# Kernel optimization log

Hardware: AMD Instinct MI355X
Metric: run time of the kernel (lower is better)

The kernel has to match this reference:

```python
import jax, jax.numpy as jnp
import numpy as np

B, H, S, D = 2, 8, 2048, 64
N_HASHES = 6
EPS = 1e-8


def setup_inputs() -> dict:
    key = jax.random.key(0)
    kq, kk, kv, kr = jax.random.split(key, 4)
    Q = jax.random.normal(kq, (B, H, S, D), dtype=jnp.float32)
    K = jax.random.normal(kk, (B, H, S, D), dtype=jnp.float32)
    V = jax.random.normal(kv, (B, H, S, D), dtype=jnp.float32)
    rotations = jax.random.normal(kr, (H, N_HASHES, D), dtype=jnp.float32)
    return {"Q": Q, "K": K, "V": V, "rotations": rotations}


def _buckets(X, rotations, powers):
    # X: [b,h,l,d] -> integer bucket id per position, [b,h,l]
    Xn = X / (jnp.linalg.norm(X, axis=-1, keepdims=True) + 1e-8)
    bits = jnp.einsum('bhld,hnd->bhln', Xn, rotations) > 0
    return jnp.sum(bits.astype(jnp.int32) * powers, axis=-1)


def reference(Q, K, V, rotations):
    n_hashes = rotations.shape[1]
    d = Q.shape[-1]
    powers = (2 ** jnp.arange(n_hashes)).astype(jnp.int32)
    q_buckets = _buckets(Q, rotations, powers)  # [b,h,sq]
    k_buckets = _buckets(K, rotations, powers)  # [b,h,sk]
    # queries only attend to keys whose full hash code matches exactly
    match = q_buckets[..., :, None] == k_buckets[..., None, :]  # [b,h,sq,sk]
    scores = jnp.einsum('bhqd,bhkd->bhqk', Q, K) / (d ** 0.5)
    row_has = jnp.any(match, axis=-1, keepdims=True)
    masked = jnp.where(match, scores, -jnp.inf)
    m = jnp.max(masked, axis=-1, keepdims=True)
    m = jnp.where(row_has, m, 0.0)  # avoid -inf for empty rows
    e = jnp.where(match, jnp.exp(scores - m), 0.0)
    weights = e / (jnp.sum(e, axis=-1, keepdims=True) + EPS)
    out = jnp.einsum('bhqk,bhkd->bhqd', weights, V)
    return out / n_hashes
```

## Files before the change

kernel.cpp:

```cpp
#include <hip/hip_runtime.h>
#include <math.h>


constexpr int S_LEN = 2048;
constexpr int D = 64;
constexpr int NHASH = 6;
constexpr int BH = 16;
constexpr int NB = 64;
constexpr int QPAD = 4;
constexpr int PADQ = S_LEN + (QPAD - 1) * NB;
constexpr int NGRP = PADQ / QPAD;
constexpr int NBLK = NGRP / 4;
constexpr int GSTRIDE = 37;
constexpr size_t KTP_OFF = 1u << 20;

__global__ __launch_bounds__(256) void lsh_buckets2(const float* __restrict__ Q,
                                                    const float* __restrict__ K,
                                                    const float* __restrict__ rot,
                                                    int* __restrict__ qb,
                                                    int* __restrict__ kb) {
    const int gw   = (blockIdx.x * 256 + threadIdx.x) >> 6;
    const int lane = threadIdx.x & 63;
    const bool isK = gw >= BH * S_LEN;
    const int wid  = isK ? gw - BH * S_LEN : gw;
    const float* X = isK ? K : Q;
    int* dst       = isK ? kb : qb;
    const int h    = (wid >> 11) & 7;

    const float x  = X[(size_t)wid * D + lane];
    const float* r = rot + (size_t)h * NHASH * D + lane;
    float p0 = x * r[0 * D], p1 = x * r[1 * D], p2 = x * r[2 * D];
    float p3 = x * r[3 * D], p4 = x * r[4 * D], p5 = x * r[5 * D];
#pragma unroll
    for (int off = 32; off >= 1; off >>= 1) {
        p0 += __shfl_xor(p0, off, 64);
        p1 += __shfl_xor(p1, off, 64);
        p2 += __shfl_xor(p2, off, 64);
        p3 += __shfl_xor(p3, off, 64);
        p4 += __shfl_xor(p4, off, 64);
        p5 += __shfl_xor(p5, off, 64);
    }
    int bucket = (p0 > 0.f ? 1 : 0) | (p1 > 0.f ? 2 : 0) | (p2 > 0.f ? 4 : 0) |
                 (p3 > 0.f ? 8 : 0) | (p4 > 0.f ? 16 : 0) | (p5 > 0.f ? 32 : 0);
    if (lane == 0) dst[wid] = bucket;
}

__global__ __launch_bounds__(256) void lsh_sortfuse_bh(const int* __restrict__ qbuckets,
                                                       const int* __restrict__ kbuckets,
                                                       int* __restrict__ q_plist,
                                                       int* __restrict__ k_list) {
    __shared__ int hist[NB];
    __shared__ int cur[NB];
    __shared__ int kst[NB], kcnt[NB];
    __shared__ int qst[NB];
    __shared__ int total;
    const int bh  = blockIdx.x;
    const int tid = threadIdx.x;

    if (tid < NB) hist[tid] = 0;
    __syncthreads();
    int myk[8];
#pragma unroll
    for (int i = 0; i < 8; ++i) {
        myk[i] = kbuckets[bh * S_LEN + i * 256 + tid];
        atomicAdd(&hist[myk[i]], 1);
    }
    __syncthreads();
    if (tid < NB) {
        const int cnt = hist[tid];
        int x = cnt;
#pragma unroll
        for (int off = 1; off < 64; off <<= 1) {
            const int y = __shfl_up(x, off, 64);
            if (tid >= off) x += y;
        }
        kst[tid]  = x - cnt;
        kcnt[tid] = cnt;
        cur[tid]  = x - cnt;
    }
    __syncthreads();
    {
        int* klp = k_list + bh * S_LEN;
#pragma unroll
        for (int i = 0; i < 8; ++i) {
            const int b    = myk[i];
            const int slot = atomicAdd(&cur[b], 1);
            klp[slot] = i * 256 + tid;
        }
    }
    __syncthreads();

    if (tid < NB) hist[tid] = 0;
    __syncthreads();
    int myq[8];
#pragma unroll
    for (int i = 0; i < 8; ++i) {
        myq[i] = qbuckets[bh * S_LEN + i * 256 + tid];
        atomicAdd(&hist[myq[i]], 1);
    }
    __syncthreads();
    if (tid < NB) {
        const int cnt = hist[tid];
        const int v   = (cnt + QPAD - 1) & ~(QPAD - 1);
        int x = v;
#pragma unroll
        for (int off = 1; off < 64; off <<= 1) {
            const int y = __shfl_up(x, off, 64);
            if (tid >= off) x += y;
        }
        qst[tid] = x - v;
        cur[tid] = x - v;
        if (tid == 63) total = x;
    }
    __syncthreads();

    int* qp = q_plist + bh * PADQ;
    if (tid < NB) {
        const int cnt    = hist[tid];
        const int padded = (cnt + QPAD - 1) & ~(QPAD - 1);
        const int sent   = 0xFFFF | (kcnt[tid] << 16);
        for (int t = qst[tid] + cnt; t < qst[tid] + padded; ++t) qp[t] = sent;
    }
    for (int t = total + tid; t < PADQ; t += 256) qp[t] = -1;
#pragma unroll
    for (int i = 0; i < 8; ++i) {
        const int b    = myq[i];
        const int slot = atomicAdd(&cur[b], 1);
        const int pos  = slot & 3;
        int e = i * 256 + tid;
        if (pos == 0)      e |= kst[b] << 16;
        else if (pos == 1) e |= kcnt[b] << 16;
        qp[slot] = e;
    }
}

__global__ __launch_bounds__(256) void lsh_kpack(const float* __restrict__ K,
                                                 const int* __restrict__ k_list,
                                                 float* __restrict__ Ktp) {
    const int gw   = (blockIdx.x * 256 + threadIdx.x) >> 6;
    const int lane = threadIdx.x & 63;
    const int bh   = gw >> 9;
    const int s0   = (gw & 511) * 4;
    const float* Kb = K + (size_t)bh * S_LEN * D;
    const int* kl   = k_list + bh * S_LEN;
    float* kt       = Ktp + (size_t)bh * 16 * S_LEN * 4;
    const int dblk  = lane >> 2, dj = lane & 3;
#pragma unroll
    for (int j = 0; j < 4; ++j) {
        const int slot = s0 + j;
        const int kidx = kl[slot];
        const float v  = Kb[(size_t)kidx * D + lane];
        kt[((size_t)dblk * S_LEN + slot) * 4 + dj] = v;
    }
}

__global__ __launch_bounds__(256) void lsh_attn_p(const float* __restrict__ Q,
                                                  const float* __restrict__ V,
                                                  const float* __restrict__ Ktp,
                                                  const int* __restrict__ q_plist,
                                                  const int* __restrict__ k_list,
                                                  float* __restrict__ out) {
    __shared__ float wbuf[4][QPAD][64];
    __shared__ int   kbuf[4][64];

    const int wv   = threadIdx.x >> 6;
    const int lane = threadIdx.x & 63;
    const int w    = blockIdx.x;
    const int bh   = (w & 7) + 8 * ((w >> 3) & 1);
    const int gb   = ((w >> 4) * GSTRIDE) % NBLK;
    const int grp  = gb * 4 + wv;

    const int* pl = q_plist + bh * PADQ + 4 * grp;
    const int e0 = __builtin_amdgcn_readfirstlane(pl[0]);
    if ((e0 & 0xFFFF) == 0xFFFF) return;
    const int e1 = __builtin_amdgcn_readfirstlane(pl[1]);
    const int e2 = __builtin_amdgcn_readfirstlane(pl[2]);
    const int e3 = __builtin_amdgcn_readfirstlane(pl[3]);

    const int q0 = e0 & 0xFFFF;
    const int ks = (unsigned)e0 >> 16;
    const int nk = (unsigned)e1 >> 16;
    const int t1 = e1 & 0xFFFF, t2 = e2 & 0xFFFF, t3 = e3 & 0xFFFF;
    const bool v1 = t1 != 0xFFFF, v2 = t2 != 0xFFFF, v3 = t3 != 0xFFFF;
    const int q1 = v1 ? t1 : q0;
    const int q2 = v2 ? t2 : q0;
    const int q3 = v3 ? t3 : q0;

    float* outb = out + (size_t)bh * S_LEN * D;
    if (nk == 0) {
        outb[(size_t)q0 * D + lane] = 0.0f;
        if (v1) outb[(size_t)q1 * D + lane] = 0.0f;
        if (v2) outb[(size_t)q2 * D + lane] = 0.0f;
        if (v3) outb[(size_t)q3 * D + lane] = 0.0f;
        return;
    }

    const int* kl     = k_list + bh * S_LEN + ks;
    const float* ktb  = Ktp + (size_t)bh * 16 * S_LEN * 4;
    const float* Vb   = V + (size_t)bh * S_LEN * D;
    const float* qr0  = Q + ((size_t)bh * S_LEN + q0) * D;
    const float* qr1  = Q + ((size_t)bh * S_LEN + q1) * D;
    const float* qr2  = Q + ((size_t)bh * S_LEN + q2) * D;
    const float* qr3  = Q + ((size_t)bh * S_LEN + q3) * D;

    float l0 = 0.f, l1 = 0.f, l2 = 0.f, l3 = 0.f;
    float acc0 = 0.f, acc1 = 0.f, acc2 = 0.f, acc3 = 0.f;

    for (int c = 0; c * 64 < nk; ++c) {
        const int cnk  = min(64, nk - c * 64);
        const int cl   = min(lane, cnk - 1);
        const int kidx = kl[c * 64 + cl];
        const int slot = ks + c * 64 + cl;

        float s0 = 0.f, s1 = 0.f, s2 = 0.f, s3 = 0.f;
#pragma unroll
        for (int d4 = 0; d4 < 16; ++d4) {
            const float4 kv = *(const float4*)(ktb + ((size_t)d4 * S_LEN + slot) * 4);
            const float4 a  = *(const float4*)(qr0 + d4 * 4);
            const float4 b  = *(const float4*)(qr1 + d4 * 4);
            const float4 cq = *(const float4*)(qr2 + d4 * 4);
            const float4 dq = *(const float4*)(qr3 + d4 * 4);
            s0 += a.x * kv.x + a.y * kv.y + a.z * kv.z + a.w * kv.w;
            s1 += b.x * kv.x + b.y * kv.y + b.z * kv.z + b.w * kv.w;
            s2 += cq.x * kv.x + cq.y * kv.y + cq.z * kv.z + cq.w * kv.w;
            s3 += dq.x * kv.x + dq.y * kv.y + dq.z * kv.z + dq.w * kv.w;
        }

        const bool kvalid = lane < cnk;
        const float ea = kvalid ? __expf(s0 * 0.125f) : 0.f;
        const float eb = kvalid ? __expf(s1 * 0.125f) : 0.f;
        const float ec = kvalid ? __expf(s2 * 0.125f) : 0.f;
        const float ed = kvalid ? __expf(s3 * 0.125f) : 0.f;
        l0 += ea; l1 += eb; l2 += ec; l3 += ed;
        wbuf[wv][0][lane] = ea;
        wbuf[wv][1][lane] = eb;
        wbuf[wv][2][lane] = ec;
        wbuf[wv][3][lane] = ed;
        kbuf[wv][lane]    = kidx;

        const int ng = (cnk + 3) >> 2;
        for (int g = 0; g < ng; ++g) {
            const int4   kk = *(const int4*)&kbuf[wv][g * 4];
            const float4 eA = *(const float4*)&wbuf[wv][0][g * 4];
            const float4 eB = *(const float4*)&wbuf[wv][1][g * 4];
            const float4 eC = *(const float4*)&wbuf[wv][2][g * 4];
            const float4 eD = *(const float4*)&wbuf[wv][3][g * 4];
            const float vx = Vb[(size_t)kk.x * D + lane];
            const float vy = Vb[(size_t)kk.y * D + lane];
            const float vz = Vb[(size_t)kk.z * D + lane];
            const float vw = Vb[(size_t)kk.w * D + lane];
            acc0 += eA.x * vx + eA.y * vy + eA.z * vz + eA.w * vw;
            acc1 += eB.x * vx + eB.y * vy + eB.z * vz + eB.w * vw;
            acc2 += eC.x * vx + eC.y * vy + eC.z * vz + eC.w * vw;
            acc3 += eD.x * vx + eD.y * vy + eD.z * vz + eD.w * vw;
        }
    }

#pragma unroll
    for (int off = 32; off >= 1; off >>= 1) {
        l0 += __shfl_xor(l0, off, 64);
        l1 += __shfl_xor(l1, off, 64);
        l2 += __shfl_xor(l2, off, 64);
        l3 += __shfl_xor(l3, off, 64);
    }

    const float inv6 = 1.0f / 6.0f;
    outb[(size_t)q0 * D + lane] = acc0 / (l0 + 1e-8f) * inv6;
    if (v1) outb[(size_t)q1 * D + lane] = acc1 / (l1 + 1e-8f) * inv6;
    if (v2) outb[(size_t)q2 * D + lane] = acc2 / (l2 + 1e-8f) * inv6;
    if (v3) outb[(size_t)q3 * D + lane] = acc3 / (l3 + 1e-8f) * inv6;
}

__global__ __launch_bounds__(256) void lsh_attn_g(const float* __restrict__ Q,
                                                  const float* __restrict__ K,
                                                  const float* __restrict__ V,
                                                  const int* __restrict__ q_plist,
                                                  const int* __restrict__ k_list,
                                                  float* __restrict__ out) {
    __shared__ float wbuf[4][QPAD][64];
    __shared__ int   kbuf[4][64];

    const int wv   = threadIdx.x >> 6;
    const int lane = threadIdx.x & 63;
    const int w    = blockIdx.x;
    const int bh   = (w & 7) + 8 * ((w >> 3) & 1);
    const int gb   = ((w >> 4) * GSTRIDE) % NBLK;
    const int grp  = gb * 4 + wv;

    const int* pl = q_plist + bh * PADQ + 4 * grp;
    const int e0 = __builtin_amdgcn_readfirstlane(pl[0]);
    if ((e0 & 0xFFFF) == 0xFFFF) return;
    const int e1 = __builtin_amdgcn_readfirstlane(pl[1]);
    const int e2 = __builtin_amdgcn_readfirstlane(pl[2]);
    const int e3 = __builtin_amdgcn_readfirstlane(pl[3]);

    const int q0 = e0 & 0xFFFF;
    const int ks = (unsigned)e0 >> 16;
    const int nk = (unsigned)e1 >> 16;
    const int t1 = e1 & 0xFFFF, t2 = e2 & 0xFFFF, t3 = e3 & 0xFFFF;
    const bool v1 = t1 != 0xFFFF, v2 = t2 != 0xFFFF, v3 = t3 != 0xFFFF;
    const int q1 = v1 ? t1 : q0;
    const int q2 = v2 ? t2 : q0;
    const int q3 = v3 ? t3 : q0;

    float* outb = out + (size_t)bh * S_LEN * D;
    if (nk == 0) {
        outb[(size_t)q0 * D + lane] = 0.0f;
        if (v1) outb[(size_t)q1 * D + lane] = 0.0f;
        if (v2) outb[(size_t)q2 * D + lane] = 0.0f;
        if (v3) outb[(size_t)q3 * D + lane] = 0.0f;
        return;
    }

    const int* kl     = k_list + bh * S_LEN + ks;
    const float* Kb   = K + (size_t)bh * S_LEN * D;
    const float* Vb   = V + (size_t)bh * S_LEN * D;
    const float* qr0  = Q + ((size_t)bh * S_LEN + q0) * D;
    const float* qr1  = Q + ((size_t)bh * S_LEN + q1) * D;
    const float* qr2  = Q + ((size_t)bh * S_LEN + q2) * D;
    const float* qr3  = Q + ((size_t)bh * S_LEN + q3) * D;

    float l0 = 0.f, l1 = 0.f, l2 = 0.f, l3 = 0.f;
    float acc0 = 0.f, acc1 = 0.f, acc2 = 0.f, acc3 = 0.f;

    for (int c = 0; c * 64 < nk; ++c) {
        const int cnk  = min(64, nk - c * 64);
        const int kidx = kl[c * 64 + min(lane, cnk - 1)];
        const float* krow = Kb + (size_t)kidx * D;

        float s0 = 0.f, s1 = 0.f, s2 = 0.f, s3 = 0.f;
#pragma unroll
        for (int d4 = 0; d4 < 16; ++d4) {
            const float4 kv = *(const float4*)(krow + d4 * 4);
            const float4 a  = *(const float4*)(qr0 + d4 * 4);
            const float4 b  = *(const float4*)(qr1 + d4 * 4);
            const float4 cq = *(const float4*)(qr2 + d4 * 4);
            const float4 dq = *(const float4*)(qr3 + d4 * 4);
            s0 += a.x * kv.x + a.y * kv.y + a.z * kv.z + a.w * kv.w;
            s1 += b.x * kv.x + b.y * kv.y + b.z * kv.z + b.w * kv.w;
            s2 += cq.x * kv.x + cq.y * kv.y + cq.z * kv.z + cq.w * kv.w;
            s3 += dq.x * kv.x + dq.y * kv.y + dq.z * kv.z + dq.w * kv.w;
        }

        const bool kvalid = lane < cnk;
        const float ea = kvalid ? __expf(s0 * 0.125f) : 0.f;
        const float eb = kvalid ? __expf(s1 * 0.125f) : 0.f;
        const float ec = kvalid ? __expf(s2 * 0.125f) : 0.f;
        const float ed = kvalid ? __expf(s3 * 0.125f) : 0.f;
        l0 += ea; l1 += eb; l2 += ec; l3 += ed;
        wbuf[wv][0][lane] = ea;
        wbuf[wv][1][lane] = eb;
        wbuf[wv][2][lane] = ec;
        wbuf[wv][3][lane] = ed;
        kbuf[wv][lane]    = kidx;

        const int ng = (cnk + 3) >> 2;
        for (int g = 0; g < ng; ++g) {
            const int4   kk = *(const int4*)&kbuf[wv][g * 4];
            const float4 eA = *(const float4*)&wbuf[wv][0][g * 4];
            const float4 eB = *(const float4*)&wbuf[wv][1][g * 4];
            const float4 eC = *(const float4*)&wbuf[wv][2][g * 4];
            const float4 eD = *(const float4*)&wbuf[wv][3][g * 4];
            const float vx = Vb[(size_t)kk.x * D + lane];
            const float vy = Vb[(size_t)kk.y * D + lane];
            const float vz = Vb[(size_t)kk.z * D + lane];
            const float vw = Vb[(size_t)kk.w * D + lane];
            acc0 += eA.x * vx + eA.y * vy + eA.z * vz + eA.w * vw;
            acc1 += eB.x * vx + eB.y * vy + eB.z * vz + eB.w * vw;
            acc2 += eC.x * vx + eC.y * vy + eC.z * vz + eC.w * vw;
            acc3 += eD.x * vx + eD.y * vy + eD.z * vz + eD.w * vw;
        }
    }

#pragma unroll
    for (int off = 32; off >= 1; off >>= 1) {
        l0 += __shfl_xor(l0, off, 64);
        l1 += __shfl_xor(l1, off, 64);
        l2 += __shfl_xor(l2, off, 64);
        l3 += __shfl_xor(l3, off, 64);
    }

    const float inv6 = 1.0f / 6.0f;
    outb[(size_t)q0 * D + lane] = acc0 / (l0 + 1e-8f) * inv6;
    if (v1) outb[(size_t)q1 * D + lane] = acc1 / (l1 + 1e-8f) * inv6;
    if (v2) outb[(size_t)q2 * D + lane] = acc2 / (l2 + 1e-8f) * inv6;
    if (v3) outb[(size_t)q3 * D + lane] = acc3 / (l3 + 1e-8f) * inv6;
}

extern "C" void kernel_launch(void* const* d_in, const int* in_sizes, int n_in,
                              void* d_out, int out_size, void* d_ws, size_t ws_size,
                              hipStream_t stream) {
    const float* Q   = (const float*)d_in[0];
    const float* K   = (const float*)d_in[1];
    const float* V   = (const float*)d_in[2];
    const float* rot = (const float*)d_in[3];
    float* out = (float*)d_out;

    char* ws = (char*)d_ws;
    int* q_buckets = (int*)(ws);
    int* k_buckets = (int*)(ws + 131072);
    int* k_list    = (int*)(ws + 262144);
    int* q_plist   = (int*)(ws + 393216);
    float* Ktp     = (float*)(ws + KTP_OFF);

    const size_t ktp_bytes = (size_t)BH * 16 * S_LEN * 4 * sizeof(float);
    const bool packed = ws_size >= KTP_OFF + ktp_bytes;

    lsh_buckets2<<<2 * BH * S_LEN / 4, 256, 0, stream>>>(Q, K, rot, q_buckets, k_buckets);
    lsh_sortfuse_bh<<<BH, 256, 0, stream>>>(q_buckets, k_buckets, q_plist, k_list);
    if (packed) {
        lsh_kpack<<<BH * S_LEN / 16, 256, 0, stream>>>(K, k_list, Ktp);
        lsh_attn_p<<<NBLK * BH, 256, 0, stream>>>(Q, V, Ktp, q_plist, k_list, out);
    } else {
        lsh_attn_g<<<NBLK * BH, 256, 0, stream>>>(Q, K, V, q_plist, k_list, out);
    }
}
```

Baseline: 72.71 us.

## Fuse bucket, sort, and K-pack kernels into one cooperative kernel

Merges the hashing, per-head counting sort, and K-packing kernels into a single cooperative launch of 1024 blocks, using grid-wide syncs between phases. The goal is to cut the launch overhead and inter-kernel gaps of three small prep kernels. In exchange, the sort phase runs on only 16 blocks while the rest wait at the grid barrier, and grid.sync itself has a cost. The cooperative launch also requires all 1024 blocks to be co-resident.

```diff
diff --git a/kernel.cpp b/kernel.cpp
--- a/kernel.cpp
+++ b/kernel.cpp
@@ -1,5 +1,8 @@
 #include <hip/hip_runtime.h>
+#include <hip/hip_cooperative_groups.h>
 #include <math.h>
+
+namespace cg = cooperative_groups;
 
 
 constexpr int S_LEN = 2048;
@@ -12,145 +15,154 @@
 constexpr int NGRP = PADQ / QPAD;
 constexpr int NBLK = NGRP / 4;
 constexpr int GSTRIDE = 37;
+constexpr int NPREP = 1024;
 constexpr size_t KTP_OFF = 1u << 20;
 
-__global__ __launch_bounds__(256) void lsh_buckets2(const float* __restrict__ Q,
-                                                    const float* __restrict__ K,
-                                                    const float* __restrict__ rot,
-                                                    int* __restrict__ qb,
-                                                    int* __restrict__ kb) {
-    const int gw   = (blockIdx.x * 256 + threadIdx.x) >> 6;
-    const int lane = threadIdx.x & 63;
-    const bool isK = gw >= BH * S_LEN;
-    const int wid  = isK ? gw - BH * S_LEN : gw;
-    const float* X = isK ? K : Q;
-    int* dst       = isK ? kb : qb;
-    const int h    = (wid >> 11) & 7;
-
-    const float x  = X[(size_t)wid * D + lane];
-    const float* r = rot + (size_t)h * NHASH * D + lane;
-    float p0 = x * r[0 * D], p1 = x * r[1 * D], p2 = x * r[2 * D];
-    float p3 = x * r[3 * D], p4 = x * r[4 * D], p5 = x * r[5 * D];
-#pragma unroll
-    for (int off = 32; off >= 1; off >>= 1) {
-        p0 += __shfl_xor(p0, off, 64);
-        p1 += __shfl_xor(p1, off, 64);
-        p2 += __shfl_xor(p2, off, 64);
-        p3 += __shfl_xor(p3, off, 64);
-        p4 += __shfl_xor(p4, off, 64);
-        p5 += __shfl_xor(p5, off, 64);
-    }
-    int bucket = (p0 > 0.f ? 1 : 0) | (p1 > 0.f ? 2 : 0) | (p2 > 0.f ? 4 : 0) |
-                 (p3 > 0.f ? 8 : 0) | (p4 > 0.f ? 16 : 0) | (p5 > 0.f ? 32 : 0);
-    if (lane == 0) dst[wid] = bucket;
-}
-
-__global__ __launch_bounds__(256) void lsh_sortfuse_bh(const int* __restrict__ qbuckets,
-                                                       const int* __restrict__ kbuckets,
-                                                       int* __restrict__ q_plist,
-                                                       int* __restrict__ k_list) {
+__global__ __launch_bounds__(256) void lsh_prep(const float* __restrict__ Q,
+                                                const float* __restrict__ K,
+                                                const float* __restrict__ rot,
+                                                int* __restrict__ qb,
+                                                int* __restrict__ kb,
+                                                int* __restrict__ q_plist,
+                                                int* __restrict__ k_list,
+                                                float* __restrict__ Ktp) {
+    cg::grid_group grid = cg::this_grid();
     __shared__ int hist[NB];
     __shared__ int cur[NB];
     __shared__ int kst[NB], kcnt[NB];
     __shared__ int qst[NB];
     __shared__ int total;
-    const int bh  = blockIdx.x;
-    const int tid = threadIdx.x;
-
-    if (tid < NB) hist[tid] = 0;
-    __syncthreads();
-    int myk[8];
-#pragma unroll
-    for (int i = 0; i < 8; ++i) {
-        myk[i] = kbuckets[bh * S_LEN + i * 256 + tid];
-        atomicAdd(&hist[myk[i]], 1);
-    }
-    __syncthreads();
-    if (tid < NB) {
-        const int cnt = hist[tid];
-        int x = cnt;
-#pragma unroll
-        for (int off = 1; off < 64; off <<= 1) {
-            const int y = __shfl_up(x, off, 64);
-            if (tid >= off) x += y;
-        }
-        kst[tid]  = x - cnt;
-        kcnt[tid] = cnt;
-        cur[tid]  = x - cnt;
-    }
-    __syncthreads();
-    {
-        int* klp = k_list + bh * S_LEN;
+
+    const int tid  = threadIdx.x;
+    const int wv   = tid >> 6;
+    const int lane = tid & 63;
+    const int wave0 = blockIdx.x * 4 + wv;
+
+    for (int it = 0; it < 16; ++it) {
+        const int gw   = wave0 + it * 4096;
+        const bool isK = gw >= BH * S_LEN;
+        const int wid  = isK ? gw - BH * S_LEN : gw;
+        const float* X = isK ? K : Q;
+        int* dst       = isK ? kb : qb;
+        const int h    = (wid >> 11) & 7;
+
+        const float x  = X[(size_t)wid * D + lane];
+        const float* r = rot + (size_t)h * NHASH * D + lane;
+        float p0 = x * r[0 * D], p1 = x * r[1 * D], p2 = x * r[2 * D];
+        float p3 = x * r[3 * D], p4 = x * r[4 * D], p5 = x * r[5 * D];
+#pragma unroll
+        for (int off = 32; off >= 1; off >>= 1) {
+            p0 += __shfl_xor(p0, off, 64);
+            p1 += __shfl_xor(p1, off, 64);
+            p2 += __shfl_xor(p2, off, 64);
+            p3 += __shfl_xor(p3, off, 64);
+            p4 += __shfl_xor(p4, off, 64);
+            p5 += __shfl_xor(p5, off, 64);
+        }
+        int bucket = (p0 > 0.f ? 1 : 0) | (p1 > 0.f ? 2 : 0) | (p2 > 0.f ? 4 : 0) |
+                     (p3 > 0.f ? 8 : 0) | (p4 > 0.f ? 16 : 0) | (p5 > 0.f ? 32 : 0);
+        if (lane == 0) dst[wid] = bucket;
+    }
+    grid.sync();
+
+    if (blockIdx.x < BH) {
+        const int bh = blockIdx.x;
+
+        if (tid < NB) hist[tid] = 0;
+        __syncthreads();
+        int myk[8];
 #pragma unroll
         for (int i = 0; i < 8; ++i) {
-            const int b    = myk[i];
+            myk[i] = kb[bh * S_LEN + i * 256 + tid];
+            atomicAdd(&hist[myk[i]], 1);
+        }
+        __syncthreads();
+        if (tid < NB) {
+            const int cnt = hist[tid];
+            int x = cnt;
+#pragma unroll
+            for (int off = 1; off < 64; off <<= 1) {
+                const int y = __shfl_up(x, off, 64);
+                if (tid >= off) x += y;
+            }
+            kst[tid]  = x - cnt;
+            kcnt[tid] = cnt;
+            cur[tid]  = x - cnt;
+        }
+        __syncthreads();
+        {
+            int* klp = k_list + bh * S_LEN;
+#pragma unroll
+            for (int i = 0; i < 8; ++i) {
+                const int b    = myk[i];
+                const int slot = atomicAdd(&cur[b], 1);
+                klp[slot] = i * 256 + tid;
+            }
+        }
+        __syncthreads();
+
+        if (tid < NB) hist[tid] = 0;
+        __syncthreads();
+        int myq[8];
+#pragma unroll
+        for (int i = 0; i < 8; ++i) {
+            myq[i] = qb[bh * S_LEN + i * 256 + tid];
+            atomicAdd(&hist[myq[i]], 1);
+        }
+        __syncthreads();
+        if (tid < NB) {
+            const int cnt = hist[tid];
+            const int v   = (cnt + QPAD - 1) & ~(QPAD - 1);
+            int x = v;
+#pragma unroll
+            for (int off = 1; off < 64; off <<= 1) {
+                const int y = __shfl_up(x, off, 64);
+                if (tid >= off) x += y;
+            }
+            qst[tid] = x - v;
+            cur[tid] = x - v;
+            if (tid == 63) total = x;
+        }
+        __syncthreads();
+
+        int* qp = q_plist + bh * PADQ;
+        if (tid < NB) {
+            const int cnt    = hist[tid];
+            const int padded = (cnt + QPAD - 1) & ~(QPAD - 1);
+            const int sent   = 0xFFFF | (kcnt[tid] << 16);
+            for (int t = qst[tid] + cnt; t < qst[tid] + padded; ++t) qp[t] = sent;
+        }
+        for (int t = total + tid; t < PADQ; t += 256) qp[t] = -1;
+#pragma unroll
+        for (int i = 0; i < 8; ++i) {
+            const int b    = myq[i];
             const int slot = atomicAdd(&cur[b], 1);
-            klp[slot] = i * 256 + tid;
-        }
-    }
-    __syncthreads();
-
-    if (tid < NB) hist[tid] = 0;
-    __syncthreads();
-    int myq[8];
-#pragma unroll
-    for (int i = 0; i < 8; ++i) {
-        myq[i] = qbuckets[bh * S_LEN + i * 256 + tid];
-        atomicAdd(&hist[myq[i]], 1);
-    }
-    __syncthreads();
-    if (tid < NB) {
-        const int cnt = hist[tid];
-        const int v   = (cnt + QPAD - 1) & ~(QPAD - 1);
-        int x = v;
-#pragma unroll
-        for (int off = 1; off < 64; off <<= 1) {
-            const int y = __shfl_up(x, off, 64);
-            if (tid >= off) x += y;
-        }
-        qst[tid] = x - v;
-        cur[tid] = x - v;
-        if (tid == 63) total = x;
-    }
-    __syncthreads();
-
-    int* qp = q_plist + bh * PADQ;
-    if (tid < NB) {
-        const int cnt    = hist[tid];
-        const int padded = (cnt + QPAD - 1) & ~(QPAD - 1);
-        const int sent   = 0xFFFF | (kcnt[tid] << 16);
-        for (int t = qst[tid] + cnt; t < qst[tid] + padded; ++t) qp[t] = sent;
-    }
-    for (int t = total + tid; t < PADQ; t += 256) qp[t] = -1;
-#pragma unroll
-    for (int i = 0; i < 8; ++i) {
-        const int b    = myq[i];
-        const int slot = atomicAdd(&cur[b], 1);
-        const int pos  = slot & 3;
-        int e = i * 256 + tid;
-        if (pos == 0)      e |= kst[b] << 16;
-        else if (pos == 1) e |= kcnt[b] << 16;
-        qp[slot] = e;
-    }
-}
-
-__global__ __launch_bounds__(256) void lsh_kpack(const float* __restrict__ K,
-                                                 const int* __restrict__ k_list,
-                                                 float* __restrict__ Ktp) {
-    const int gw   = (blockIdx.x * 256 + threadIdx.x) >> 6;
-    const int lane = threadIdx.x & 63;
-    const int bh   = gw >> 9;
-    const int s0   = (gw & 511) * 4;
-    const float* Kb = K + (size_t)bh * S_LEN * D;
-    const int* kl   = k_list + bh * S_LEN;
-    float* kt       = Ktp + (size_t)bh * 16 * S_LEN * 4;
-    const int dblk  = lane >> 2, dj = lane & 3;
-#pragma unroll
-    for (int j = 0; j < 4; ++j) {
-        const int slot = s0 + j;
-        const int kidx = kl[slot];
-        const float v  = Kb[(size_t)kidx * D + lane];
-        kt[((size_t)dblk * S_LEN + slot) * 4 + dj] = v;
+            const int pos  = slot & 3;
+            int e = i * 256 + tid;
+            if (pos == 0)      e |= kst[b] << 16;
+            else if (pos == 1) e |= kcnt[b] << 16;
+            qp[slot] = e;
+        }
+    }
+    grid.sync();
+
+    if (Ktp != nullptr) {
+        for (int it = 0; it < 2; ++it) {
+            const int gw = wave0 + it * 4096;
+            const int bh = gw >> 9;
+            const int s0 = (gw & 511) * 4;
+            const float* Kb = K + (size_t)bh * S_LEN * D;
+            const int* kl   = k_list + bh * S_LEN;
+            float* kt       = Ktp + (size_t)bh * 16 * S_LEN * 4;
+            const int dblk  = lane >> 2, dj = lane & 3;
+#pragma unroll
+            for (int j = 0; j < 4; ++j) {
+                const int slot = s0 + j;
+                const int kidx = kl[slot];
+                const float v  = Kb[(size_t)kidx * D + lane];
+                kt[((size_t)dblk * S_LEN + slot) * 4 + dj] = v;
+            }
+        }
     }
 }
 
@@ -401,15 +413,20 @@
     int* k_buckets = (int*)(ws + 131072);
     int* k_list    = (int*)(ws + 262144);
     int* q_plist   = (int*)(ws + 393216);
-    float* Ktp     = (float*)(ws + KTP_OFF);
 
     const size_t ktp_bytes = (size_t)BH * 16 * S_LEN * 4 * sizeof(float);
     const bool packed = ws_size >= KTP_OFF + ktp_bytes;
-
-    lsh_buckets2<<<2 * BH * S_LEN / 4, 256, 0, stream>>>(Q, K, rot, q_buckets, k_buckets);
-    lsh_sortfuse_bh<<<BH, 256, 0, stream>>>(q_buckets, k_buckets, q_plist, k_list);
+    float* Ktp = packed ? (float*)(ws + KTP_OFF) : nullptr;
+
+    const float* Qa = Q; const float* Ka = K; const float* rota = rot;
+    int* qba = q_buckets; int* kba = k_buckets;
+    int* qpa = q_plist;   int* kla = k_list;
+    float* kta = Ktp;
+    void* args[] = {(void*)&Qa, (void*)&Ka, (void*)&rota, (void*)&qba, (void*)&kba,
+                    (void*)&qpa, (void*)&kla, (void*)&kta};
+    hipLaunchCooperativeKernel((void*)lsh_prep, dim3(NPREP), dim3(256), args, 0, stream);
+
     if (packed) {
-        lsh_kpack<<<BH * S_LEN / 16, 256, 0, stream>>>(K, k_list, Ktp);
         lsh_attn_p<<<NBLK * BH, 256, 0, stream>>>(Q, V, Ktp, q_plist, k_list, out);
     } else {
         lsh_attn_g<<<NBLK * BH, 256, 0, stream>>>(Q, K, V, q_plist, k_list, out);
```

Result: slower. 277.9 us (+282.1%).

## Pack V in bucket order, split sort across 32 blocks, use 1024-thread hashing

Applied to the files above, without the earlier changes.

The pack kernel now gathers V rows into bucket-sorted order alongside K, so the attention kernel reads contiguous V rows instead of gathering through k_list and a shared-memory index buffer. The sort kernel is split so 16 blocks build the key list while 16 others compute key counts and the padded query list in parallel. The hashing kernel also moves to 1024-thread blocks. The cost is an extra full copy of V written to workspace, and the packed path now needs a larger workspace or it falls back to the gather path.

```diff
diff --git a/kernel.cpp b/kernel.cpp
--- a/kernel.cpp
+++ b/kernel.cpp
@@ -13,13 +13,14 @@
 constexpr int NBLK = NGRP / 4;
 constexpr int GSTRIDE = 37;
 constexpr size_t KTP_OFF = 1u << 20;
-
-__global__ __launch_bounds__(256) void lsh_buckets2(const float* __restrict__ Q,
-                                                    const float* __restrict__ K,
-                                                    const float* __restrict__ rot,
-                                                    int* __restrict__ qb,
-                                                    int* __restrict__ kb) {
-    const int gw   = (blockIdx.x * 256 + threadIdx.x) >> 6;
+constexpr size_t VTP_OFF = KTP_OFF + ((size_t)BH * 16 * S_LEN * 4 * 4);
+
+__global__ __launch_bounds__(1024) void lsh_buckets2(const float* __restrict__ Q,
+                                                     const float* __restrict__ K,
+                                                     const float* __restrict__ rot,
+                                                     int* __restrict__ qb,
+                                                     int* __restrict__ kb) {
+    const int gw   = blockIdx.x * 16 + (threadIdx.x >> 6);
     const int lane = threadIdx.x & 63;
     const bool isK = gw >= BH * S_LEN;
     const int wid  = isK ? gw - BH * S_LEN : gw;
@@ -45,41 +46,40 @@
     if (lane == 0) dst[wid] = bucket;
 }
 
-__global__ __launch_bounds__(256) void lsh_sortfuse_bh(const int* __restrict__ qbuckets,
-                                                       const int* __restrict__ kbuckets,
-                                                       int* __restrict__ q_plist,
-                                                       int* __restrict__ k_list) {
+__global__ __launch_bounds__(256) void lsh_sortfuse32(const int* __restrict__ qbuckets,
+                                                      const int* __restrict__ kbuckets,
+                                                      int* __restrict__ q_plist,
+                                                      int* __restrict__ k_list) {
     __shared__ int hist[NB];
     __shared__ int cur[NB];
     __shared__ int kst[NB], kcnt[NB];
     __shared__ int qst[NB];
     __shared__ int total;
-    const int bh  = blockIdx.x;
-    const int tid = threadIdx.x;
-
-    if (tid < NB) hist[tid] = 0;
-    __syncthreads();
-    int myk[8];
-#pragma unroll
-    for (int i = 0; i < 8; ++i) {
-        myk[i] = kbuckets[bh * S_LEN + i * 256 + tid];
-        atomicAdd(&hist[myk[i]], 1);
-    }
-    __syncthreads();
-    if (tid < NB) {
-        const int cnt = hist[tid];
-        int x = cnt;
-#pragma unroll
-        for (int off = 1; off < 64; off <<= 1) {
-            const int y = __shfl_up(x, off, 64);
-            if (tid >= off) x += y;
-        }
-        kst[tid]  = x - cnt;
-        kcnt[tid] = cnt;
-        cur[tid]  = x - cnt;
-    }
-    __syncthreads();
-    {
+    const int which = blockIdx.x >> 4;
+    const int bh    = blockIdx.x & 15;
+    const int tid   = threadIdx.x;
+
+    if (which) {
+        if (tid < NB) hist[tid] = 0;
+        __syncthreads();
+        int myk[8];
+#pragma unroll
+        for (int i = 0; i < 8; ++i) {
+            myk[i] = kbuckets[bh * S_LEN + i * 256 + tid];
+            atomicAdd(&hist[myk[i]], 1);
+        }
+        __syncthreads();
+        if (tid < NB) {
+            const int cnt = hist[tid];
+            int x = cnt;
+#pragma unroll
+            for (int off = 1; off < 64; off <<= 1) {
+                const int y = __shfl_up(x, off, 64);
+                if (tid >= off) x += y;
+            }
+            cur[tid] = x - cnt;
+        }
+        __syncthreads();
         int* klp = k_list + bh * S_LEN;
 #pragma unroll
         for (int i = 0; i < 8; ++i) {
@@ -87,81 +87,101 @@
             const int slot = atomicAdd(&cur[b], 1);
             klp[slot] = i * 256 + tid;
         }
-    }
-    __syncthreads();
-
-    if (tid < NB) hist[tid] = 0;
-    __syncthreads();
-    int myq[8];
-#pragma unroll
-    for (int i = 0; i < 8; ++i) {
-        myq[i] = qbuckets[bh * S_LEN + i * 256 + tid];
-        atomicAdd(&hist[myq[i]], 1);
-    }
-    __syncthreads();
-    if (tid < NB) {
-        const int cnt = hist[tid];
-        const int v   = (cnt + QPAD - 1) & ~(QPAD - 1);
-        int x = v;
-#pragma unroll
-        for (int off = 1; off < 64; off <<= 1) {
-            const int y = __shfl_up(x, off, 64);
-            if (tid >= off) x += y;
-        }
-        qst[tid] = x - v;
-        cur[tid] = x - v;
-        if (tid == 63) total = x;
-    }
-    __syncthreads();
-
-    int* qp = q_plist + bh * PADQ;
-    if (tid < NB) {
-        const int cnt    = hist[tid];
-        const int padded = (cnt + QPAD - 1) & ~(QPAD - 1);
-        const int sent   = 0xFFFF | (kcnt[tid] << 16);
-        for (int t = qst[tid] + cnt; t < qst[tid] + padded; ++t) qp[t] = sent;
-    }
-    for (int t = total + tid; t < PADQ; t += 256) qp[t] = -1;
-#pragma unroll
-    for (int i = 0; i < 8; ++i) {
-        const int b    = myq[i];
-        const int slot = atomicAdd(&cur[b], 1);
-        const int pos  = slot & 3;
-        int e = i * 256 + tid;
-        if (pos == 0)      e |= kst[b] << 16;
-        else if (pos == 1) e |= kcnt[b] << 16;
-        qp[slot] = e;
-    }
-}
-
-__global__ __launch_bounds__(256) void lsh_kpack(const float* __restrict__ K,
-                                                 const int* __restrict__ k_list,
-                                                 float* __restrict__ Ktp) {
+    } else {
+        if (tid < NB) hist[tid] = 0;
+        __syncthreads();
+#pragma unroll
+        for (int i = 0; i < 8; ++i)
+            atomicAdd(&hist[kbuckets[bh * S_LEN + i * 256 + tid]], 1);
+        __syncthreads();
+        if (tid < NB) {
+            const int cnt = hist[tid];
+            int x = cnt;
+#pragma unroll
+            for (int off = 1; off < 64; off <<= 1) {
+                const int y = __shfl_up(x, off, 64);
+                if (tid >= off) x += y;
+            }
+            kst[tid]  = x - cnt;
+            kcnt[tid] = cnt;
+        }
+        __syncthreads();
+
+        if (tid < NB) hist[tid] = 0;
+        __syncthreads();
+        int myq[8];
+#pragma unroll
+        for (int i = 0; i < 8; ++i) {
+            myq[i] = qbuckets[bh * S_LEN + i * 256 + tid];
+            atomicAdd(&hist[myq[i]], 1);
+        }
+        __syncthreads();
+        if (tid < NB) {
+            const int cnt = hist[tid];
+            const int v   = (cnt + QPAD - 1) & ~(QPAD - 1);
+            int x = v;
+#pragma unroll
+            for (int off = 1; off < 64; off <<= 1) {
+                const int y = __shfl_up(x, off, 64);
+                if (tid >= off) x += y;
+            }
+            qst[tid] = x - v;
+            cur[tid] = x - v;
+            if (tid == 63) total = x;
+        }
+        __syncthreads();
+
+        int* qp = q_plist + bh * PADQ;
+        if (tid < NB) {
+            const int cnt    = hist[tid];
+            const int padded = (cnt + QPAD - 1) & ~(QPAD - 1);
+            const int sent   = 0xFFFF | (kcnt[tid] << 16);
+            for (int t = qst[tid] + cnt; t < qst[tid] + padded; ++t) qp[t] = sent;
+        }
+        for (int t = total + tid; t < PADQ; t += 256) qp[t] = -1;
+#pragma unroll
+        for (int i = 0; i < 8; ++i) {
+            const int b    = myq[i];
+            const int slot = atomicAdd(&cur[b], 1);
+            const int pos  = slot & 3;
+            int e = i * 256 + tid;
+            if (pos == 0)      e |= kst[b] << 16;
+            else if (pos == 1) e |= kcnt[b] << 16;
+            qp[slot] = e;
+        }
+    }
+}
+
+__global__ __launch_bounds__(256) void lsh_packkv(const float* __restrict__ K,
+                                                  const float* __restrict__ V,
+                                                  const int* __restrict__ k_list,
+                                                  float* __restrict__ Ktp,
+                                                  float* __restrict__ Vtp) {
     const int gw   = (blockIdx.x * 256 + threadIdx.x) >> 6;
     const int lane = threadIdx.x & 63;
     const int bh   = gw >> 9;
     const int s0   = (gw & 511) * 4;
     const float* Kb = K + (size_t)bh * S_LEN * D;
+    const float* Vb = V + (size_t)bh * S_LEN * D;
     const int* kl   = k_list + bh * S_LEN;
     float* kt       = Ktp + (size_t)bh * 16 * S_LEN * 4;
+    float* vt       = Vtp + (size_t)bh * S_LEN * D;
     const int dblk  = lane >> 2, dj = lane & 3;
 #pragma unroll
     for (int j = 0; j < 4; ++j) {
         const int slot = s0 + j;
         const int kidx = kl[slot];
-        const float v  = Kb[(size_t)kidx * D + lane];
-        kt[((size_t)dblk * S_LEN + slot) * 4 + dj] = v;
-    }
-}
-
-__global__ __launch_bounds__(256) void lsh_attn_p(const float* __restrict__ Q,
-                                                  const float* __restrict__ V,
-                                                  const float* __restrict__ Ktp,
-                                                  const int* __restrict__ q_plist,
-                                                  const int* __restrict__ k_list,
-                                                  float* __restrict__ out) {
+        kt[((size_t)dblk * S_LEN + slot) * 4 + dj] = Kb[(size_t)kidx * D + lane];
+        vt[(size_t)slot * D + lane]                = Vb[(size_t)kidx * D + lane];
+    }
+}
+
+__global__ __launch_bounds__(256) void lsh_attn_pv(const float* __restrict__ Q,
+                                                   const float* __restrict__ Ktp,
+                                                   const float* __restrict__ Vtp,
+                                                   const int* __restrict__ q_plist,
+                                                   float* __restrict__ out) {
     __shared__ float wbuf[4][QPAD][64];
-    __shared__ int   kbuf[4][64];
 
     const int wv   = threadIdx.x >> 6;
     const int lane = threadIdx.x & 63;
@@ -195,8 +215,122 @@
         return;
     }
 
+    const float* ktb  = Ktp + (size_t)bh * 16 * S_LEN * 4;
+    const float* vtb  = Vtp + (size_t)bh * S_LEN * D;
+    const float* qr0  = Q + ((size_t)bh * S_LEN + q0) * D;
+    const float* qr1  = Q + ((size_t)bh * S_LEN + q1) * D;
+    const float* qr2  = Q + ((size_t)bh * S_LEN + q2) * D;
+    const float* qr3  = Q + ((size_t)bh * S_LEN + q3) * D;
+
+    float l0 = 0.f, l1 = 0.f, l2 = 0.f, l3 = 0.f;
+    float acc0 = 0.f, acc1 = 0.f, acc2 = 0.f, acc3 = 0.f;
+
+    for (int c = 0; c * 64 < nk; ++c) {
+        const int cnk  = min(64, nk - c * 64);
+        const int cl   = min(lane, cnk - 1);
+        const int slot = ks + c * 64 + cl;
+
+        float s0 = 0.f, s1 = 0.f, s2 = 0.f, s3 = 0.f;
+#pragma unroll
+        for (int d4 = 0; d4 < 16; ++d4) {
+            const float4 kv = *(const float4*)(ktb + ((size_t)d4 * S_LEN + slot) * 4);
+            const float4 a  = *(const float4*)(qr0 + d4 * 4);
+            const float4 b  = *(const float4*)(qr1 + d4 * 4);
+            const float4 cq = *(const float4*)(qr2 + d4 * 4);
+            const float4 dq = *(const float4*)(qr3 + d4 * 4);
+            s0 += a.x * kv.x + a.y * kv.y + a.z * kv.z + a.w * kv.w;
+            s1 += b.x * kv.x + b.y * kv.y + b.z * kv.z + b.w * kv.w;
+            s2 += cq.x * kv.x + cq.y * kv.y + cq.z * kv.z + cq.w * kv.w;
+            s3 += dq.x * kv.x + dq.y * kv.y + dq.z * kv.z + dq.w * kv.w;
+        }
+
+        const bool kvalid = lane < cnk;
+        const float ea = kvalid ? __expf(s0 * 0.125f) : 0.f;
+        const float eb = kvalid ? __expf(s1 * 0.125f) : 0.f;
+        const float ec = kvalid ? __expf(s2 * 0.125f) : 0.f;
+        const float ed = kvalid ? __expf(s3 * 0.125f) : 0.f;
+        l0 += ea; l1 += eb; l2 += ec; l3 += ed;
+        wbuf[wv][0][lane] = ea;
+        wbuf[wv][1][lane] = eb;
+        wbuf[wv][2][lane] = ec;
+        wbuf[wv][3][lane] = ed;
+
+        const float* vrow = vtb + (size_t)(ks + c * 64) * D;
+        const int ng = (cnk + 3) >> 2;
+        for (int g = 0; g < ng; ++g) {
+            const float4 eA = *(const float4*)&wbuf[wv][0][g * 4];
+            const float4 eB = *(const float4*)&wbuf[wv][1][g * 4];
+            const float4 eC = *(const float4*)&wbuf[wv][2][g * 4];
+            const float4 eD = *(const float4*)&wbuf[wv][3][g * 4];
+            const float vx = vrow[(g * 4 + 0) * D + lane];
+            const float vy = vrow[(g * 4 + 1) * D + lane];
+            const float vz = vrow[(g * 4 + 2) * D + lane];
+            const float vw = vrow[(g * 4 + 3) * D + lane];
+            acc0 += eA.x * vx + eA.y * vy + eA.z * vz + eA.w * vw;
+            acc1 += eB.x * vx + eB.y * vy + eB.z * vz + eB.w * vw;
+            acc2 += eC.x * vx + eC.y * vy + eC.z * vz + eC.w * vw;
+            acc3 += eD.x * vx + eD.y * vy + eD.z * vz + eD.w * vw;
+        }
+    }
+
+#pragma unroll
+    for (int off = 32; off >= 1; off >>= 1) {
+        l0 += __shfl_xor(l0, off, 64);
+        l1 += __shfl_xor(l1, off, 64);
+        l2 += __shfl_xor(l2, off, 64);
+        l3 += __shfl_xor(l3, off, 64);
+    }
+
+    const float inv6 = 1.0f / 6.0f;
+    outb[(size_t)q0 * D + lane] = acc0 / (l0 + 1e-8f) * inv6;
+    if (v1) outb[(size_t)q1 * D + lane] = acc1 / (l1 + 1e-8f) * inv6;
+    if (v2) outb[(size_t)q2 * D + lane] = acc2 / (l2 + 1e-8f) * inv6;
+    if (v3) outb[(size_t)q3 * D + lane] = acc3 / (l3 + 1e-8f) * inv6;
+}
+
+__global__ __launch_bounds__(256) void lsh_attn_g(const float* __restrict__ Q,
+                                                  const float* __restrict__ K,
+                                                  const float* __restrict__ V,
+                                                  const int* __restrict__ q_plist,
+                                                  const int* __restrict__ k_list,
+                                                  float* __restrict__ out) {
+    __shared__ float wbuf[4][QPAD][64];
+    __shared__ int   kbuf[4][64];
+
+    const int wv   = threadIdx.x >> 6;
+    const int lane = threadIdx.x & 63;
+    const int w    = blockIdx.x;
+    const int bh   = (w & 7) + 8 * ((w >> 3) & 1);
+    const int gb   = ((w >> 4) * GSTRIDE) % NBLK;
+    const int grp  = gb * 4 + wv;
+
+    const int* pl = q_plist + bh * PADQ + 4 * grp;
+    const int e0 = __builtin_amdgcn_readfirstlane(pl[0]);
+    if ((e0 & 0xFFFF) == 0xFFFF) return;
+    const int e1 = __builtin_amdgcn_readfirstlane(pl[1]);
+    const int e2 = __builtin_amdgcn_readfirstlane(pl[2]);
+    const int e3 = __builtin_amdgcn_readfirstlane(pl[3]);
+
+    const int q0 = e0 & 0xFFFF;
+    const int ks = (unsigned)e0 >> 16;
+    const int nk = (unsigned)e1 >> 16;
+    const int t1 = e1 & 0xFFFF, t2 = e2 & 0xFFFF, t3 = e3 & 0xFFFF;
+    const bool v1 = t1 != 0xFFFF, v2 = t2 != 0xFFFF, v3 = t3 != 0xFFFF;
+    const int q1 = v1 ? t1 : q0;
+    const int q2 = v2 ? t2 : q0;
+    const int q3 = v3 ? t3 : q0;
+
+    float* outb = out + (size_t)bh * S_LEN * D;
+    if (nk == 0) {
+        outb[(size_t)q0 * D + lane] = 0.0f;
+        if (v1) outb[(size_t)q1 * D + lane] = 0.0f;
+        if (v2) outb[(size_t)q2 * D + lane] = 0.0f;
+        if (v3) outb[(size_t)q3 * D + lane] = 0.0f;
+        return;
+    }
+
     const int* kl     = k_list + bh * S_LEN + ks;
-    const float* ktb  = Ktp + (size_t)bh * 16 * S_LEN * 4;
+    const float* Kb   = K + (size_t)bh * S_LEN * D;
     const float* Vb   = V + (size_t)bh * S_LEN * D;
     const float* qr0  = Q + ((size_t)bh * S_LEN + q0) * D;
     const float* qr1  = Q + ((size_t)bh * S_LEN + q1) * D;
@@ -208,14 +342,13 @@
 
     for (int c = 0; c * 64 < nk; ++c) {
         const int cnk  = min(64, nk - c * 64);
-        const int cl   = min(lane, cnk - 1);
-        const int kidx = kl[c * 64 + cl];
-        const int slot = ks + c * 64 + cl;
+        const int kidx = kl[c * 64 + min(lane, cnk - 1)];
+        const float* krow = Kb + (size_t)kidx * D;
 
         float s0 = 0.f, s1 = 0.f, s2 = 0.f, s3 = 0.f;
 #pragma unroll
         for (int d4 = 0; d4 < 16; ++d4) {
-            const float4 kv = *(const float4*)(ktb + ((size_t)d4 * S_LEN + slot) * 4);
+            const float4 kv = *(const float4*)(krow + d4 * 4);
             const float4 a  = *(const float4*)(qr0 + d4 * 4);
             const float4 b  = *(const float4*)(qr1 + d4 * 4);
             const float4 cq = *(const float4*)(qr2 + d4 * 4);
@@ -271,122 +404,6 @@
     if (v3) outb[(size_t)q3 * D + lane] = acc3 / (l3 + 1e-8f) * inv6;
 }
 
-__global__ __launch_bounds__(256) void lsh_attn_g(const float* __restrict__ Q,
-                                                  const float* __restrict__ K,
-                                                  const float* __restrict__ V,
-                                                  const int* __restrict__ q_plist,
-                                                  const int* __restrict__ k_list,
-                                                  float* __restrict__ out) {
-    __shared__ float wbuf[4][QPAD][64];
-    __shared__ int   kbuf[4][64];
-
-    const int wv   = threadIdx.x >> 6;
-    const int lane = threadIdx.x & 63;
-    const int w    = blockIdx.x;
-    const int bh   = (w & 7) + 8 * ((w >> 3) & 1);
-    const int gb   = ((w >> 4) * GSTRIDE) % NBLK;
-    const int grp  = gb * 4 + wv;
-
-    const int* pl = q_plist + bh * PADQ + 4 * grp;
-    const int e0 = __builtin_amdgcn_readfirstlane(pl[0]);
-    if ((e0 & 0xFFFF) == 0xFFFF) return;
-    const int e1 = __builtin_amdgcn_readfirstlane(pl[1]);
-    const int e2 = __builtin_amdgcn_readfirstlane(pl[2]);
-    const int e3 = __builtin_amdgcn_readfirstlane(pl[3]);
-
-    const int q0 = e0 & 0xFFFF;
-    const int ks = (unsigned)e0 >> 16;
-    const int nk = (unsigned)e1 >> 16;
-    const int t1 = e1 & 0xFFFF, t2 = e2 & 0xFFFF, t3 = e3 & 0xFFFF;
-    const bool v1 = t1 != 0xFFFF, v2 = t2 != 0xFFFF, v3 = t3 != 0xFFFF;
-    const int q1 = v1 ? t1 : q0;
-    const int q2 = v2 ? t2 : q0;
-    const int q3 = v3 ? t3 : q0;
-
-    float* outb = out + (size_t)bh * S_LEN * D;
-    if (nk == 0) {
-        outb[(size_t)q0 * D + lane] = 0.0f;
-        if (v1) outb[(size_t)q1 * D + lane] = 0.0f;
-        if (v2) outb[(size_t)q2 * D + lane] = 0.0f;
-        if (v3) outb[(size_t)q3 * D + lane] = 0.0f;
-        return;
-    }
-
-    const int* kl     = k_list + bh * S_LEN + ks;
-    const float* Kb   = K + (size_t)bh * S_LEN * D;
-    const float* Vb   = V + (size_t)bh * S_LEN * D;
-    const float* qr0  = Q + ((size_t)bh * S_LEN + q0) * D;
-    const float* qr1  = Q + ((size_t)bh * S_LEN + q1) * D;
-    const float* qr2  = Q + ((size_t)bh * S_LEN + q2) * D;
-    const float* qr3  = Q + ((size_t)bh * S_LEN + q3) * D;
-
-    float l0 = 0.f, l1 = 0.f, l2 = 0.f, l3 = 0.f;
-    float acc0 = 0.f, acc1 = 0.f, acc2 = 0.f, acc3 = 0.f;
-
-    for (int c = 0; c * 64 < nk; ++c) {
-        const int cnk  = min(64, nk - c * 64);
-        const int kidx = kl[c * 64 + min(lane, cnk - 1)];
-        const float* krow = Kb + (size_t)kidx * D;
-
-        float s0 = 0.f, s1 = 0.f, s2 = 0.f, s3 = 0.f;
-#pragma unroll
-        for (int d4 = 0; d4 < 16; ++d4) {
-            const float4 kv = *(const float4*)(krow + d4 * 4);
-            const float4 a  = *(const float4*)(qr0 + d4 * 4);
-            const float4 b  = *(const float4*)(qr1 + d4 * 4);
-            const float4 cq = *(const float4*)(qr2 + d4 * 4);
-            const float4 dq = *(const float4*)(qr3 + d4 * 4);
-            s0 += a.x * kv.x + a.y * kv.y + a.z * kv.z + a.w * kv.w;
-            s1 += b.x * kv.x + b.y * kv.y + b.z * kv.z + b.w * kv.w;
-            s2 += cq.x * kv.x + cq.y * kv.y + cq.z * kv.z + cq.w * kv.w;
-            s3 += dq.x * kv.x + dq.y * kv.y + dq.z * kv.z + dq.w * kv.w;
-        }
-
-        const bool kvalid = lane < cnk;
-        const float ea = kvalid ? __expf(s0 * 0.125f) : 0.f;
-        const float eb = kvalid ? __expf(s1 * 0.125f) : 0.f;
-        const float ec = kvalid ? __expf(s2 * 0.125f) : 0.f;
-        const float ed = kvalid ? __expf(s3 * 0.125f) : 0.f;
-        l0 += ea; l1 += eb; l2 += ec; l3 += ed;
-        wbuf[wv][0][lane] = ea;
-        wbuf[wv][1][lane] = eb;
-        wbuf[wv][2][lane] = ec;
-        wbuf[wv][3][lane] = ed;
-        kbuf[wv][lane]    = kidx;
-
-        const int ng = (cnk + 3) >> 2;
-        for (int g = 0; g < ng; ++g) {
-            const int4   kk = *(const int4*)&kbuf[wv][g * 4];
-            const float4 eA = *(const float4*)&wbuf[wv][0][g * 4];
-            const float4 eB = *(const float4*)&wbuf[wv][1][g * 4];
-            const float4 eC = *(const float4*)&wbuf[wv][2][g * 4];
-            const float4 eD = *(const float4*)&wbuf[wv][3][g * 4];
-            const float vx = Vb[(size_t)kk.x * D + lane];
-            const float vy = Vb[(size_t)kk.y * D + lane];
-            const float vz = Vb[(size_t)kk.z * D + lane];
-            const float vw = Vb[(size_t)kk.w * D + lane];
-            acc0 += eA.x * vx + eA.y * vy + eA.z * vz + eA.w * vw;
-            acc1 += eB.x * vx + eB.y * vy + eB.z * vz + eB.w * vw;
-            acc2 += eC.x * vx + eC.y * vy + eC.z * vz + eC.w * vw;
-            acc3 += eD.x * vx + eD.y * vy + eD.z * vz + eD.w * vw;
-        }
-    }
-
-#pragma unroll
-    for (int off = 32; off >= 1; off >>= 1) {
-        l0 += __shfl_xor(l0, off, 64);
-        l1 += __shfl_xor(l1, off, 64);
-        l2 += __shfl_xor(l2, off, 64);
-        l3 += __shfl_xor(l3, off, 64);
-    }
-
-    const float inv6 = 1.0f / 6.0f;
-    outb[(size_t)q0 * D + lane] = acc0 / (l0 + 1e-8f) * inv6;
-    if (v1) outb[(size_t)q1 * D + lane] = acc1 / (l1 + 1e-8f) * inv6;
-    if (v2) outb[(size_t)q2 * D + lane] = acc2 / (l2 + 1e-8f) * inv6;
-    if (v3) outb[(size_t)q3 * D + lane] = acc3 / (l3 + 1e-8f) * inv6;
-}
-
 extern "C" void kernel_launch(void* const* d_in, const int* in_sizes, int n_in,
                               void* d_out, int out_size, void* d_ws, size_t ws_size,
                               hipStream_t stream) {
@@ -401,16 +418,17 @@
     int* k_buckets = (int*)(ws + 131072);
     int* k_list    = (int*)(ws + 262144);
     int* q_plist   = (int*)(ws + 393216);
-    float* Ktp     = (float*)(ws + KTP_OFF);
-
-    const size_t ktp_bytes = (size_t)BH * 16 * S_LEN * 4 * sizeof(float);
-    const bool packed = ws_size >= KTP_OFF + ktp_bytes;
-
-    lsh_buckets2<<<2 * BH * S_LEN / 4, 256, 0, stream>>>(Q, K, rot, q_buckets, k_buckets);
-    lsh_sortfuse_bh<<<BH, 256, 0, stream>>>(q_buckets, k_buckets, q_plist, k_list);
+
+    const size_t pack_bytes = (size_t)BH * S_LEN * D * sizeof(float);
+    const bool packed = ws_size >= VTP_OFF + pack_bytes + 16384;
+    float* Ktp = (float*)(ws + KTP_OFF);
+    float* Vtp = (float*)(ws + VTP_OFF);
+
+    lsh_buckets2<<<2 * BH * S_LEN / 16, 1024, 0, stream>>>(Q, K, rot, q_buckets, k_buckets);
+    lsh_sortfuse32<<<32, 256, 0, stream>>>(q_buckets, k_buckets, q_plist, k_list);
     if (packed) {
-        lsh_kpack<<<BH * S_LEN / 16, 256, 0, stream>>>(K, k_list, Ktp);
-        lsh_attn_p<<<NBLK * BH, 256, 0, stream>>>(Q, V, Ktp, q_plist, k_list, out);
+        lsh_packkv<<<BH * S_LEN / 16, 256, 0, stream>>>(K, V, k_list, Ktp, Vtp);
+        lsh_attn_pv<<<NBLK * BH, 256, 0, stream>>>(Q, Ktp, Vtp, q_plist, out);
     } else {
         lsh_attn_g<<<NBLK * BH, 256, 0, stream>>>(Q, K, V, q_plist, k_list, out);
     }
```

Measured after the change: 74.85 us. 2.9% more time.
